# Performance work log

Hardware: AMD Instinct MI355X
Metric: run time of the kernel (lower is better)

## Reference

```python
import jax, jax.numpy as jnp
import numpy as np

B, T, H, E = 4, 8192, 512, 2048  # batch, seq, hidden (num_dims), embed (num_embeds)
LN_EPS = 1e-5


def _layernorm(x, g, b):
    m = x.mean(-1, keepdims=True)
    v = ((x - m) ** 2).mean(-1, keepdims=True)
    return (x - m) * jax.lax.rsqrt(v + LN_EPS) * g + b


def setup_inputs() -> dict:
    key = jax.random.key(0)
    ks = jax.random.split(key, 8)
    C = 64
    tri = jnp.tril(jnp.ones((C, C), jnp.float32))
    kw = 1.0 / np.sqrt(C)
    inp = {
        "x": jax.random.normal(ks[0], (B, T, H), jnp.float32),
        "ln1_g": jnp.ones((H,), jnp.float32),
        "ln1_b": jnp.zeros((H,), jnp.float32),
        # TriLinear weights: (features, features), lower-triangular masked at init
        "W1": jax.random.uniform(ks[1], (C, C), jnp.float32, -kw, kw) * tri,
        "W2": jax.random.uniform(ks[2], (C, C), jnp.float32, -kw, kw) * tri,
        "ln2_g": jnp.ones((H,), jnp.float32),
        "ln2_b": jnp.zeros((H,), jnp.float32),
        # ffw: Linear(H->E), sin, Linear(E->H); stored (in, out)
        "fw1": jax.random.uniform(ks[3], (H, E), jnp.float32, -1.0 / np.sqrt(H), 1.0 / np.sqrt(H)),
        "fb1": jax.random.uniform(ks[4], (E,), jnp.float32, -1.0 / np.sqrt(H), 1.0 / np.sqrt(H)),
        "fw2": jax.random.uniform(ks[5], (E, H), jnp.float32, -1.0 / np.sqrt(E), 1.0 / np.sqrt(E)),
        "fb2": jax.random.uniform(ks[6], (H,), jnp.float32, -1.0 / np.sqrt(E), 1.0 / np.sqrt(E)),
        "chunk_size": 64,
        "stride": 32,
    }
    return inp


def reference(x, ln1_g, ln1_b, W1, W2, ln2_g, ln2_b, fw1, fb1, fw2, fb2, chunk_size, stride):
    Bb, Tt, Hh = x.shape
    C = chunk_size
    starts = jnp.arange(0, Tt, stride)              # (N,)
    pos = starts[:, None] + jnp.arange(C)           # (N, C)
    valid = (pos < Tt)
    vmask = valid[None, :, :, None].astype(x.dtype)
    safe = jnp.minimum(pos, Tt - 1)
    chunks = x[:, safe] * vmask                     # (B, N, C, H): padded chunks (zeros past T)
    resid = chunks
    cn = _layernorm(chunks, ln1_g, ln1_b)
    tri = jnp.tril(jnp.ones((C, C), x.dtype))
    # TriLinear on time axis (torch transposes to (B,H,C); einsum avoids the transpose)
    y = jnp.einsum('ts,bnsh->bnth', W1 * tri, cn)
    y = jnp.einsum('ts,bnsh->bnth', W2 * tri, y)
    c2 = y + resid
    h = _layernorm(c2, ln2_g, ln2_b)
    h = jnp.sin(h @ fw1 + fb1) @ fw2 + fb2
    out_chunks = (h + c2) * vmask                   # zero the padded tail (torch truncates it)
    flat = safe.reshape(-1)                         # (N*C,)
    out = jnp.zeros_like(x).at[:, flat].add(out_chunks.reshape(Bb, -1, Hh))
    counts = jnp.zeros((Tt,), x.dtype).at[flat].add(valid.reshape(-1).astype(x.dtype))
    return out / jnp.maximum(counts, 1.0)[None, :, None]
```

## Files before the change

### kernel.cpp

```cpp
#include <hip/hip_runtime.h>
#include <math.h>

#define TB 4
#define TT 8192
#define TH 512
#define TE 2048
#define NCHUNK 256
#define GCTOT 1024

typedef unsigned short u16;
typedef short bf8v __attribute__((ext_vector_type(8)));
typedef float f4v __attribute__((ext_vector_type(4)));

__device__ __forceinline__ float bu2f(u16 u) {
    unsigned int x = ((unsigned int)u) << 16; float f; __builtin_memcpy(&f, &x, 4); return f;
}
__device__ __forceinline__ u16 f2bu(float f) {
    unsigned int x; __builtin_memcpy(&x, &f, 4);
    x = x + 0x7fffu + ((x >> 16) & 1u);
    return (u16)(x >> 16);
}

__global__ __launch_bounds__(256) void make_Mt(const float* __restrict__ W1,
                                               const float* __restrict__ W2,
                                               float* __restrict__ Mt) {
    __shared__ float w1[64 * 64];
    __shared__ float w2[64 * 64];
    for (int i = threadIdx.x; i < 4096; i += 256) { w1[i] = W1[i]; w2[i] = W2[i]; }
    __syncthreads();
    for (int i = threadIdx.x; i < 4096; i += 256) {
        int t = i >> 6, s = i & 63;
        float a = 0.f;
        if (t >= s) for (int k = s; k <= t; ++k) a += w2[t * 64 + k] * w1[k * 64 + s];
        Mt[s * 64 + t] = a;
    }
}

__global__ __launch_bounds__(256) void transpose_b(const float* __restrict__ in,
                                                   u16* __restrict__ out, int R, int C) {
    __shared__ u16 tile[64][65];
    const int bx = blockIdx.x, by = blockIdx.y;
    const int tx = threadIdx.x & 63, ty = threadIdx.x >> 6;
#pragma unroll
    for (int i = 0; i < 16; ++i) {
        int r = ty + i * 4;
        tile[r][tx] = f2bu(in[(size_t)(by * 64 + r) * C + bx * 64 + tx]);
    }
    __syncthreads();
#pragma unroll
    for (int i = 0; i < 16; ++i) {
        int r = ty + i * 4;
        out[(size_t)(bx * 64 + r) * R + by * 64 + tx] = tile[tx][r];
    }
}

__global__ __launch_bounds__(256) void ln_stats(const float* __restrict__ x,
                                                float2* __restrict__ st) {
    const int wave = threadIdx.x >> 6, lane = threadIdx.x & 63;
    const size_t row = (size_t)blockIdx.x * 4 + wave;
    const float4* p = (const float4*)(x + row * TH);
    float4 a = p[lane * 2], b = p[lane * 2 + 1];
    float s = 0.f, q = 0.f;
    float v[8] = {a.x, a.y, a.z, a.w, b.x, b.y, b.z, b.w};
#pragma unroll
    for (int i = 0; i < 8; ++i) { s += v[i]; q += v[i] * v[i]; }
#pragma unroll
    for (int o = 32; o; o >>= 1) { s += __shfl_xor(s, o); q += __shfl_xor(q, o); }
    const float mean = s * (1.f / TH);
    float var = q * (1.f / TH) - mean * mean;
    if (var < 0.f) var = 0.f;
    if (lane == 0) st[row] = make_float2(mean, rsqrtf(var + 1e-5f));
}

__global__ __launch_bounds__(256) void ln_rows(const u16* __restrict__ in,
                                               u16* __restrict__ out,
                                               const float* __restrict__ g,
                                               const float* __restrict__ b) {
    const int wave = threadIdx.x >> 6, lane = threadIdx.x & 63;
    const size_t row = (size_t)blockIdx.x * 4 + wave;
    uint4 raw = *((const uint4*)(in + row * TH) + lane);
    const u16* e = (const u16*)&raw;
    float v[8]; float s = 0.f, q = 0.f;
#pragma unroll
    for (int i = 0; i < 8; ++i) { v[i] = bu2f(e[i]); s += v[i]; q += v[i] * v[i]; }
#pragma unroll
    for (int o = 32; o; o >>= 1) { s += __shfl_xor(s, o); q += __shfl_xor(q, o); }
    const float mean = s * (1.f / TH);
    float var = q * (1.f / TH) - mean * mean;
    if (var < 0.f) var = 0.f;
    const float rstd = rsqrtf(var + 1e-5f);
    float4 g0 = ((const float4*)g)[lane * 2], g1 = ((const float4*)g)[lane * 2 + 1];
    float4 b0 = ((const float4*)b)[lane * 2], b1 = ((const float4*)b)[lane * 2 + 1];
    float ge[8] = {g0.x, g0.y, g0.z, g0.w, g1.x, g1.y, g1.z, g1.w};
    float be[8] = {b0.x, b0.y, b0.z, b0.w, b1.x, b1.y, b1.z, b1.w};
    u16 ov[8];
#pragma unroll
    for (int i = 0; i < 8; ++i) ov[i] = f2bu((v[i] - mean) * rstd * ge[i] + be[i]);
    *((uint4*)(out + row * TH) + lane) = *(uint4*)ov;
}

__global__ __launch_bounds__(256) void trilinear_f(const float* __restrict__ x,
                                                   const float2* __restrict__ st,
                                                   const float* __restrict__ g,
                                                   const float* __restrict__ bb,
                                                   const float* __restrict__ Mt,
                                                   u16* __restrict__ c2s,
                                                   int gc0) {
    const int ln = blockIdx.x;
    const int gc = gc0 + ln;
    const int b = gc >> 8, n = gc & 255;
    const int h = (blockIdx.y << 8) + threadIdx.x;
    const int base = n * 32;
    const float gh = g[h], bh = bb[h];
    float acc[64];
#pragma unroll
    for (int t = 0; t < 64; ++t) acc[t] = 0.f;
    for (int s = 0; s < 64; ++s) {
        int pos = base + s; if (pos > TT - 1) pos = TT - 1;
        const size_t ro = (size_t)b * TT + pos;
        const float2 mr = st[ro];
        const float cn = (x[ro * TH + h] - mr.x) * mr.y * gh + bh;
        const float* m = Mt + s * 64;
#pragma unroll
        for (int t = 0; t < 64; ++t) acc[t] += m[t] * cn;
    }
#pragma unroll
    for (int t = 0; t < 64; ++t) {
        int pos = base + t; if (pos > TT - 1) pos = TT - 1;
        const float resid = x[((size_t)b * TT + pos) * TH + h];
        c2s[(size_t)(ln * 64 + t) * TH + h] = f2bu(acc[t] + resid);
    }
}

template <int MODE>
__global__ __launch_bounds__(512, 2) void gemm_w(const u16* __restrict__ A,
                                                 const u16* __restrict__ Bt,
                                                 u16* __restrict__ C,
                                                 const float* __restrict__ bias,
                                                 const u16* __restrict__ addp,
                                                 int N, int K) {
    __shared__ __attribute__((aligned(16))) u16 lA[2][256 * 64];
    __shared__ __attribute__((aligned(16))) u16 lB[2][256 * 64];
    const int tid = threadIdx.x;
    const int wave = tid >> 6;
    const int lane = tid & 63;
    const int wr = wave >> 2;
    const int wc = wave & 3;
    const int fr = lane & 15;
    const int fq = (lane >> 4) << 3;
    const int s8 = (fr & 7) << 3;

    int bx = blockIdx.x, by = blockIdx.y;
    const int gx = gridDim.x;
    const int nwg = gx * (int)gridDim.y;
    if ((nwg & 7) == 0) {
        const int bid = by * gx + bx;
        const int swz = (bid & 7) * (nwg >> 3) + (bid >> 3);
        bx = swz % gx; by = swz / gx;
    }
    const int bm = by << 8;
    const int bn = bx << 8;

    const int srow = tid >> 3;
    const int gch = ((tid & 7) ^ (srow & 7)) << 3;
    const u16* pa = A + (size_t)(bm + srow) * K + gch;
    const u16* pb = Bt + (size_t)(bn + srow) * K + gch;
    const int ldsw = wave << 9;

    const int NT = K >> 6;
    f4v acc[8][4] = {};

    auto stage = [&](int t, int buf) {
        const size_t ko = (size_t)t << 6;
#pragma unroll
        for (int i = 0; i < 4; ++i)
            __builtin_amdgcn_global_load_lds(
                (const __attribute__((address_space(1))) void*)(pa + (size_t)(i * 64) * K + ko),
                (__attribute__((address_space(3))) void*)(&lA[buf][(i << 12) + ldsw]), 16, 0, 0);
#pragma unroll
        for (int i = 0; i < 4; ++i)
            __builtin_amdgcn_global_load_lds(
                (const __attribute__((address_space(1))) void*)(pb + (size_t)(i * 64) * K + ko),
                (__attribute__((address_space(3))) void*)(&lB[buf][(i << 12) + ldsw]), 16, 0, 0);
    };

    stage(0, 0);
    stage(1, 1);
    asm volatile("s_waitcnt vmcnt(8)" ::: "memory");
    asm volatile("s_barrier" ::: "memory");

    const int arow0 = (wr << 7) + fr;
    const int brow0 = (wc << 6) + fr;
    const int c0 = fq ^ s8;
    const int c1 = (32 + fq) ^ s8;

    for (int t = 0; t < NT; ++t) {
        const int buf = t & 1;
        const u16* la = lA[buf];
        const u16* lb = lB[buf];
        bf8v af[8][2], bf[4][2];
#pragma unroll
        for (int mi = 0; mi < 8; ++mi) {
            af[mi][0] = *(const bf8v*)(la + ((arow0 + (mi << 4)) << 6) + c0);
            af[mi][1] = *(const bf8v*)(la + ((arow0 + (mi << 4)) << 6) + c1);
        }
#pragma unroll
        for (int ni = 0; ni < 4; ++ni) {
            bf[ni][0] = *(const bf8v*)(lb + ((brow0 + (ni << 4)) << 6) + c0);
            bf[ni][1] = *(const bf8v*)(lb + ((brow0 + (ni << 4)) << 6) + c1);
        }
        asm volatile("s_waitcnt lgkmcnt(0)" ::: "memory");
        __builtin_amdgcn_sched_barrier(0);
        asm volatile("s_barrier" ::: "memory");
        if (t + 2 < NT) stage(t + 2, buf);
        __builtin_amdgcn_s_setprio(1);
#pragma unroll
        for (int ks = 0; ks < 2; ++ks)
#pragma unroll
            for (int mi = 0; mi < 8; ++mi)
#pragma unroll
                for (int ni = 0; ni < 4; ++ni)
                    acc[mi][ni] = __builtin_amdgcn_mfma_f32_16x16x32_bf16(af[mi][ks], bf[ni][ks], acc[mi][ni], 0, 0, 0);
        __builtin_amdgcn_s_setprio(0);
        if (t + 1 < NT) {
            if (t + 2 < NT) asm volatile("s_waitcnt vmcnt(8)" ::: "memory");
            else            asm volatile("s_waitcnt vmcnt(0)" ::: "memory");
            asm volatile("s_barrier" ::: "memory");
        }
    }

    const int rq = (lane >> 4) << 2;
#pragma unroll
    for (int mi = 0; mi < 8; ++mi) {
#pragma unroll
        for (int ni = 0; ni < 4; ++ni) {
            const int col = bn + (wc << 6) + (ni << 4) + fr;
            const float bv = bias[col];
#pragma unroll
            for (int r = 0; r < 4; ++r) {
                const int row = bm + (wr << 7) + (mi << 4) + rq + r;
                float v = acc[mi][ni][r] + bv;
                if (MODE == 1) v = __sinf(v);
                else v += bu2f(addp[(size_t)row * N + col]);
                C[(size_t)row * N + col] = f2bu(v);
            }
        }
    }
}

template <int MODE>
__global__ __launch_bounds__(256) void gemm_db(const u16* __restrict__ A,
                                               const u16* __restrict__ Bt,
                                               u16* __restrict__ C,
                                               const float* __restrict__ bias,
                                               const u16* __restrict__ addp,
                                               int N, int K) {
    __shared__ __attribute__((aligned(16))) u16 lA[2][128 * 64];
    __shared__ __attribute__((aligned(16))) u16 lB[2][128 * 64];
    const int tid = threadIdx.x;
    const int wave = tid >> 6;
    const int lane = tid & 63;
    const int wr = wave >> 1;
    const int wc = wave & 1;
    const int fr = lane & 15;
    const int fq = (lane >> 4) << 3;
    const int s8 = (fr & 7) << 3;

    int bx = blockIdx.x, by = blockIdx.y;
    const int gx = gridDim.x;
    const int nwg = gx * (int)gridDim.y;
    if ((nwg & 7) == 0) {
        const int bid = by * gx + bx;
        const int swz = (bid & 7) * (nwg >> 3) + (bid >> 3);
        bx = swz % gx; by = swz / gx;
    }
    const int bm = by << 7;
    const int bn = bx << 7;

    const int srow = tid >> 3;
    const int gch = ((tid & 7) ^ (srow & 7)) << 3;
    const u16* pa = A + (size_t)(bm + srow) * K + gch;
    const u16* pb = Bt + (size_t)(bn + srow) * K + gch;
    const int ldsw = wave << 9;

    const int NT = K >> 6;
    f4v acc[4][4] = {};

    auto stage = [&](int t, int buf) {
        const int ko = t << 6;
#pragma unroll
        for (int i = 0; i < 4; ++i) {
            __builtin_amdgcn_global_load_lds(
                (const __attribute__((address_space(1))) void*)(pa + (size_t)(i * 32) * K + ko),
                (__attribute__((address_space(3))) void*)(&lA[buf][(i << 11) + ldsw]), 16, 0, 0);
            __builtin_amdgcn_global_load_lds(
                (const __attribute__((address_space(1))) void*)(pb + (size_t)(i * 32) * K + ko),
                (__attribute__((address_space(3))) void*)(&lB[buf][(i << 11) + ldsw]), 16, 0, 0);
        }
    };

    stage(0, 0);
    __syncthreads();

    const int arow0 = (wr << 6) + fr;
    const int brow0 = (wc << 6) + fr;
    const int c0 = fq ^ s8;
    const int c1 = (32 + fq) ^ s8;

    int buf = 0;
    for (int t = 0; t < NT; ++t) {
        if (t + 1 < NT) stage(t + 1, buf ^ 1);
        const u16* la = lA[buf];
        const u16* lb = lB[buf];
#pragma unroll
        for (int half = 0; half < 2; ++half) {
            const int cc = half ? c1 : c0;
            bf8v af[4], bfv[4];
#pragma unroll
            for (int mi = 0; mi < 4; ++mi)
                af[mi] = *(const bf8v*)(la + ((arow0 + (mi << 4)) << 6) + cc);
#pragma unroll
            for (int ni = 0; ni < 4; ++ni)
                bfv[ni] = *(const bf8v*)(lb + ((brow0 + (ni << 4)) << 6) + cc);
#pragma unroll
            for (int mi = 0; mi < 4; ++mi)
#pragma unroll
                for (int ni = 0; ni < 4; ++ni)
                    acc[mi][ni] = __builtin_amdgcn_mfma_f32_16x16x32_bf16(af[mi], bfv[ni], acc[mi][ni], 0, 0, 0);
        }
        __syncthreads();
        buf ^= 1;
    }

    const int rq = (lane >> 4) << 2;
#pragma unroll
    for (int mi = 0; mi < 4; ++mi) {
#pragma unroll
        for (int ni = 0; ni < 4; ++ni) {
            const int col = bn + (wc << 6) + (ni << 4) + fr;
            const float bv = bias[col];
#pragma unroll
            for (int r = 0; r < 4; ++r) {
                const int row = bm + (wr << 6) + (mi << 4) + rq + r;
                float v = acc[mi][ni][r] + bv;
                if (MODE == 1) v = __sinf(v);
                else v += bu2f(addp[(size_t)row * N + col]);
                C[(size_t)row * N + col] = f2bu(v);
            }
        }
    }
}

__global__ __launch_bounds__(256) void gather_slice(const u16* __restrict__ ocs,
                                                    const u16* __restrict__ carry,
                                                    float* __restrict__ out,
                                                    int gc0) {
    const int idx = blockIdx.x * 256 + threadIdx.x;
    const int h8 = idx & 63;
    const int prow = idx >> 6;
    const int ap = gc0 * 32 + prow;
    const int b = ap >> 13, t = ap & 8191;
    const int n = t >> 5, c = t & 31;
    const int ln = (b << 8) + n - gc0;
    uint4 r1 = *((const uint4*)ocs + (size_t)(ln * 64 + c) * 64 + h8);
    const u16* e1 = (const u16*)&r1;
    float ov[8];
    if (t < 32) {
#pragma unroll
        for (int i = 0; i < 8; ++i) ov[i] = bu2f(e1[i]);
    } else {
        uint4 r0;
        if (ln == 0) r0 = *((const uint4*)carry + (size_t)(c + 32) * 64 + h8);
        else         r0 = *((const uint4*)ocs + (size_t)((ln - 1) * 64 + c + 32) * 64 + h8);
        const u16* e0 = (const u16*)&r0;
#pragma unroll
        for (int i = 0; i < 8; ++i) ov[i] = 0.5f * (bu2f(e1[i]) + bu2f(e0[i]));
    }
    float4* dst = (float4*)(out + (size_t)ap * TH + h8 * 8);
    dst[0] = make_float4(ov[0], ov[1], ov[2], ov[3]);
    dst[1] = make_float4(ov[4], ov[5], ov[6], ov[7]);
}

__global__ __launch_bounds__(256) void save_carry(const u16* __restrict__ ocs,
                                                  u16* __restrict__ carry, int SC) {
    const int i = blockIdx.x * 256 + threadIdx.x;
    ((uint4*)carry)[i] = ((const uint4*)(ocs + (size_t)(SC - 1) * 64 * TH))[i];
}

extern "C" void kernel_launch(void* const* d_in, const int* in_sizes, int n_in,
                              void* d_out, int out_size, void* d_ws, size_t ws_size,
                              hipStream_t stream) {
    const float* x   = (const float*)d_in[0];
    const float* g1  = (const float*)d_in[1];
    const float* b1  = (const float*)d_in[2];
    const float* W1  = (const float*)d_in[3];
    const float* W2  = (const float*)d_in[4];
    const float* g2  = (const float*)d_in[5];
    const float* b2  = (const float*)d_in[6];
    const float* fw1 = (const float*)d_in[7];
    const float* fb1 = (const float*)d_in[8];
    const float* fw2 = (const float*)d_in[9];
    const float* fb2 = (const float*)d_in[10];
    float* out = (float*)d_out;
    char* ws = (char*)d_ws;

    size_t o = 0;
    auto take = [&](size_t n) { size_t r = o; o = (o + n + 255) & ~(size_t)255; return r; };
    float*  Mt    = (float*) (ws + take(64 * 64 * 4));
    u16*    f1t   = (u16*)   (ws + take((size_t)TE * TH * 2));
    u16*    f2t   = (u16*)   (ws + take((size_t)TH * TE * 2));
    float2* st1   = (float2*)(ws + take((size_t)TB * TT * 8));
    u16*    carry = (u16*)   (ws + take((size_t)64 * TH * 2));
    const size_t fixed = o;

    int SC = 4;
    for (int cand = 256; cand >= 4; cand >>= 1) {
        size_t per = (size_t)cand * 64 * (TH * 2 * 3 + TE * 2) + 4 * 256;
        if (fixed + per <= ws_size) { SC = cand; break; }
    }
    u16* c2s = (u16*)(ws + take((size_t)SC * 64 * TH * 2));
    u16* h2s = (u16*)(ws + take((size_t)SC * 64 * TH * 2));
    u16* ocs = (u16*)(ws + take((size_t)SC * 64 * TH * 2));
    u16* us  = (u16*)(ws + take((size_t)SC * 64 * TE * 2));
    const int SR = SC * 64;

    make_Mt<<<1, 256, 0, stream>>>(W1, W2, Mt);
    transpose_b<<<dim3(TE / 64, TH / 64), 256, 0, stream>>>(fw1, f1t, TH, TE);
    transpose_b<<<dim3(TH / 64, TE / 64), 256, 0, stream>>>(fw2, f2t, TE, TH);
    ln_stats<<<(TB * TT) / 4, 256, 0, stream>>>(x, st1);

    for (int gc0 = 0; gc0 < GCTOT; gc0 += SC) {
        trilinear_f<<<dim3(SC, TH / 256), 256, 0, stream>>>(x, st1, g1, b1, Mt, c2s, gc0);
        ln_rows<<<SR / 4, 256, 0, stream>>>(c2s, h2s, g2, b2);
        gemm_w<1><<<dim3(TE / 256, SR / 256), 512, 0, stream>>>(
            h2s, f1t, us, fb1, (const u16*)nullptr, TE, TH);
        gemm_db<2><<<dim3(TH / 128, SR / 128), 256, 0, stream>>>(
            us, f2t, ocs, fb2, c2s, TH, TE);
        gather_slice<<<SC * 8, 256, 0, stream>>>(ocs, carry, out, gc0);
        save_carry<<<16, 256, 0, stream>>>(ocs, carry, SC);
    }
}
```

Measured before the change: 692.4 us.

## Fuse LN1 stats, trilinear and LN2 into one kernel; merge carry save into gather

Drops the separate ln_stats and ln_rows kernels. A new tri_ln block handles a whole chunk with 512 threads: it loads x once into registers, computes the LN1 statistics with block reductions, does the trilinear mix, adds the residual and computes LN2 in place, writing both c2s and h2s. The carry copy is folded into gather_slice as extra blocks, using double-buffered carry slots to avoid a read/write race. This cuts launches and the global reads of x and c2s, in exchange for heavy register pressure (xv[64] plus acc[64] per thread) and fewer, larger blocks per slice.

Result: slower. 801.2 us (+15.7%).

```diff
diff --git a/kernel.cpp b/kernel.cpp
--- a/kernel.cpp
+++ b/kernel.cpp
@@ -54,82 +54,85 @@
     }
 }
 
-__global__ __launch_bounds__(256) void ln_stats(const float* __restrict__ x,
-                                                float2* __restrict__ st) {
-    const int wave = threadIdx.x >> 6, lane = threadIdx.x & 63;
-    const size_t row = (size_t)blockIdx.x * 4 + wave;
-    const float4* p = (const float4*)(x + row * TH);
-    float4 a = p[lane * 2], b = p[lane * 2 + 1];
-    float s = 0.f, q = 0.f;
-    float v[8] = {a.x, a.y, a.z, a.w, b.x, b.y, b.z, b.w};
-#pragma unroll
-    for (int i = 0; i < 8; ++i) { s += v[i]; q += v[i] * v[i]; }
-#pragma unroll
-    for (int o = 32; o; o >>= 1) { s += __shfl_xor(s, o); q += __shfl_xor(q, o); }
-    const float mean = s * (1.f / TH);
-    float var = q * (1.f / TH) - mean * mean;
-    if (var < 0.f) var = 0.f;
-    if (lane == 0) st[row] = make_float2(mean, rsqrtf(var + 1e-5f));
-}
-
-__global__ __launch_bounds__(256) void ln_rows(const u16* __restrict__ in,
-                                               u16* __restrict__ out,
-                                               const float* __restrict__ g,
-                                               const float* __restrict__ b) {
-    const int wave = threadIdx.x >> 6, lane = threadIdx.x & 63;
-    const size_t row = (size_t)blockIdx.x * 4 + wave;
-    uint4 raw = *((const uint4*)(in + row * TH) + lane);
-    const u16* e = (const u16*)&raw;
-    float v[8]; float s = 0.f, q = 0.f;
-#pragma unroll
-    for (int i = 0; i < 8; ++i) { v[i] = bu2f(e[i]); s += v[i]; q += v[i] * v[i]; }
-#pragma unroll
-    for (int o = 32; o; o >>= 1) { s += __shfl_xor(s, o); q += __shfl_xor(q, o); }
-    const float mean = s * (1.f / TH);
-    float var = q * (1.f / TH) - mean * mean;
-    if (var < 0.f) var = 0.f;
-    const float rstd = rsqrtf(var + 1e-5f);
-    float4 g0 = ((const float4*)g)[lane * 2], g1 = ((const float4*)g)[lane * 2 + 1];
-    float4 b0 = ((const float4*)b)[lane * 2], b1 = ((const float4*)b)[lane * 2 + 1];
-    float ge[8] = {g0.x, g0.y, g0.z, g0.w, g1.x, g1.y, g1.z, g1.w};
-    float be[8] = {b0.x, b0.y, b0.z, b0.w, b1.x, b1.y, b1.z, b1.w};
-    u16 ov[8];
-#pragma unroll
-    for (int i = 0; i < 8; ++i) ov[i] = f2bu((v[i] - mean) * rstd * ge[i] + be[i]);
-    *((uint4*)(out + row * TH) + lane) = *(uint4*)ov;
-}
-
-__global__ __launch_bounds__(256) void trilinear_f(const float* __restrict__ x,
-                                                   const float2* __restrict__ st,
-                                                   const float* __restrict__ g,
-                                                   const float* __restrict__ bb,
-                                                   const float* __restrict__ Mt,
-                                                   u16* __restrict__ c2s,
-                                                   int gc0) {
+__global__ __launch_bounds__(512) void tri_ln(const float* __restrict__ x,
+                                              const float* __restrict__ g1v,
+                                              const float* __restrict__ b1v,
+                                              const float* __restrict__ Mt,
+                                              const float* __restrict__ g2v,
+                                              const float* __restrict__ b2v,
+                                              u16* __restrict__ c2s,
+                                              u16* __restrict__ h2s,
+                                              int gc0) {
+    __shared__ float red[64][8][2];
+    __shared__ float2 ms[64];
     const int ln = blockIdx.x;
     const int gc = gc0 + ln;
     const int b = gc >> 8, n = gc & 255;
-    const int h = (blockIdx.y << 8) + threadIdx.x;
+    const int h = threadIdx.x;
+    const int wave = h >> 6, lane = h & 63;
     const int base = n * 32;
-    const float gh = g[h], bh = bb[h];
+
+    float xv[64];
+#pragma unroll
+    for (int s = 0; s < 64; ++s) {
+        int pos = base + s; if (pos > TT - 1) pos = TT - 1;
+        xv[s] = x[((size_t)b * TT + pos) * TH + h];
+    }
+#pragma unroll
+    for (int s = 0; s < 64; ++s) {
+        float s1 = xv[s], s2 = xv[s] * xv[s];
+#pragma unroll
+        for (int o = 32; o; o >>= 1) { s1 += __shfl_xor(s1, o); s2 += __shfl_xor(s2, o); }
+        if (lane == 0) { red[s][wave][0] = s1; red[s][wave][1] = s2; }
+    }
+    __syncthreads();
+    if (h < 64) {
+        float s1 = 0.f, s2 = 0.f;
+#pragma unroll
+        for (int w = 0; w < 8; ++w) { s1 += red[h][w][0]; s2 += red[h][w][1]; }
+        const float mean = s1 * (1.f / TH);
+        float var = s2 * (1.f / TH) - mean * mean;
+        if (var < 0.f) var = 0.f;
+        ms[h] = make_float2(mean, rsqrtf(var + 1e-5f));
+    }
+    __syncthreads();
+
+    const float gh = g1v[h], bh = b1v[h];
     float acc[64];
 #pragma unroll
     for (int t = 0; t < 64; ++t) acc[t] = 0.f;
     for (int s = 0; s < 64; ++s) {
-        int pos = base + s; if (pos > TT - 1) pos = TT - 1;
-        const size_t ro = (size_t)b * TT + pos;
-        const float2 mr = st[ro];
-        const float cn = (x[ro * TH + h] - mr.x) * mr.y * gh + bh;
+        const float cn = (xv[s] - ms[s].x) * ms[s].y * gh + bh;
         const float* m = Mt + s * 64;
 #pragma unroll
         for (int t = 0; t < 64; ++t) acc[t] += m[t] * cn;
     }
+    __syncthreads();
+
 #pragma unroll
     for (int t = 0; t < 64; ++t) {
-        int pos = base + t; if (pos > TT - 1) pos = TT - 1;
-        const float resid = x[((size_t)b * TT + pos) * TH + h];
-        c2s[(size_t)(ln * 64 + t) * TH + h] = f2bu(acc[t] + resid);
-    }
+        acc[t] += xv[t];
+        c2s[(size_t)(ln * 64 + t) * TH + h] = f2bu(acc[t]);
+        float s1 = acc[t], s2 = acc[t] * acc[t];
+#pragma unroll
+        for (int o = 32; o; o >>= 1) { s1 += __shfl_xor(s1, o); s2 += __shfl_xor(s2, o); }
+        if (lane == 0) { red[t][wave][0] = s1; red[t][wave][1] = s2; }
+    }
+    __syncthreads();
+    if (h < 64) {
+        float s1 = 0.f, s2 = 0.f;
+#pragma unroll
+        for (int w = 0; w < 8; ++w) { s1 += red[h][w][0]; s2 += red[h][w][1]; }
+        const float mean = s1 * (1.f / TH);
+        float var = s2 * (1.f / TH) - mean * mean;
+        if (var < 0.f) var = 0.f;
+        ms[h] = make_float2(mean, rsqrtf(var + 1e-5f));
+    }
+    __syncthreads();
+    const float g2h = g2v[h], b2h = b2v[h];
+#pragma unroll
+    for (int t = 0; t < 64; ++t)
+        h2s[(size_t)(ln * 64 + t) * TH + h] = f2bu((acc[t] - ms[t].x) * ms[t].y * g2h + b2h);
 }
 
 template <int MODE>
@@ -352,9 +355,15 @@
 }
 
 __global__ __launch_bounds__(256) void gather_slice(const u16* __restrict__ ocs,
-                                                    const u16* __restrict__ carry,
+                                                    const u16* __restrict__ cin,
+                                                    u16* __restrict__ cout,
                                                     float* __restrict__ out,
-                                                    int gc0) {
+                                                    int gc0, int SC) {
+    if ((int)blockIdx.x >= (SC << 3)) {
+        const int i = ((int)blockIdx.x - (SC << 3)) * 256 + threadIdx.x;
+        ((uint4*)cout)[i] = ((const uint4*)(ocs + (size_t)(SC - 1) * 64 * TH))[i];
+        return;
+    }
     const int idx = blockIdx.x * 256 + threadIdx.x;
     const int h8 = idx & 63;
     const int prow = idx >> 6;
@@ -370,7 +379,7 @@
         for (int i = 0; i < 8; ++i) ov[i] = bu2f(e1[i]);
     } else {
         uint4 r0;
-        if (ln == 0) r0 = *((const uint4*)carry + (size_t)(c + 32) * 64 + h8);
+        if (ln == 0) r0 = *((const uint4*)cin + (size_t)(c + 32) * 64 + h8);
         else         r0 = *((const uint4*)ocs + (size_t)((ln - 1) * 64 + c + 32) * 64 + h8);
         const u16* e0 = (const u16*)&r0;
 #pragma unroll
@@ -379,12 +388,6 @@
     float4* dst = (float4*)(out + (size_t)ap * TH + h8 * 8);
     dst[0] = make_float4(ov[0], ov[1], ov[2], ov[3]);
     dst[1] = make_float4(ov[4], ov[5], ov[6], ov[7]);
-}
-
-__global__ __launch_bounds__(256) void save_carry(const u16* __restrict__ ocs,
-                                                  u16* __restrict__ carry, int SC) {
-    const int i = blockIdx.x * 256 + threadIdx.x;
-    ((uint4*)carry)[i] = ((const uint4*)(ocs + (size_t)(SC - 1) * 64 * TH))[i];
 }
 
 extern "C" void kernel_launch(void* const* d_in, const int* in_sizes, int n_in,
@@ -409,8 +412,7 @@
     float*  Mt    = (float*) (ws + take(64 * 64 * 4));
     u16*    f1t   = (u16*)   (ws + take((size_t)TE * TH * 2));
     u16*    f2t   = (u16*)   (ws + take((size_t)TH * TE * 2));
-    float2* st1   = (float2*)(ws + take((size_t)TB * TT * 8));
-    u16*    carry = (u16*)   (ws + take((size_t)64 * TH * 2));
+    u16*    carry = (u16*)   (ws + take((size_t)2 * 64 * TH * 2));
     const size_t fixed = o;
 
     int SC = 4;
@@ -427,16 +429,16 @@
     make_Mt<<<1, 256, 0, stream>>>(W1, W2, Mt);
     transpose_b<<<dim3(TE / 64, TH / 64), 256, 0, stream>>>(fw1, f1t, TH, TE);
     transpose_b<<<dim3(TH / 64, TE / 64), 256, 0, stream>>>(fw2, f2t, TE, TH);
-    ln_stats<<<(TB * TT) / 4, 256, 0, stream>>>(x, st1);
-
-    for (int gc0 = 0; gc0 < GCTOT; gc0 += SC) {
-        trilinear_f<<<dim3(SC, TH / 256), 256, 0, stream>>>(x, st1, g1, b1, Mt, c2s, gc0);
-        ln_rows<<<SR / 4, 256, 0, stream>>>(c2s, h2s, g2, b2);
+
+    int si = 0;
+    for (int gc0 = 0; gc0 < GCTOT; gc0 += SC, ++si) {
+        tri_ln<<<SC, 512, 0, stream>>>(x, g1, b1, Mt, g2, b2, c2s, h2s, gc0);
         gemm_w<1><<<dim3(TE / 256, SR / 256), 512, 0, stream>>>(
             h2s, f1t, us, fb1, (const u16*)nullptr, TE, TH);
         gemm_db<2><<<dim3(TH / 128, SR / 128), 256, 0, stream>>>(
             us, f2t, ocs, fb2, c2s, TH, TE);
-        gather_slice<<<SC * 8, 256, 0, stream>>>(ocs, carry, out, gc0);
-        save_carry<<<16, 256, 0, stream>>>(ocs, carry, SC);
-    }
-}
+        u16* cin  = carry + (size_t)(si & 1) * 64 * TH;
+        u16* cout = carry + (size_t)((si + 1) & 1) * 64 * TH;
+        gather_slice<<<SC * 8 + 16, 256, 0, stream>>>(ocs, cin, cout, out, gc0, SC);
+    }
+}
```
